# Kernel optimization log

Measured on AMD Instinct MI355X. Metric: run time of the kernel, lower is better.

## Reference

```python
import jax, jax.numpy as jnp
import numpy as np

N = 50000      # nodes
E = 400000     # edges (before self-loops)
IN = 128       # in_channels
H = 4          # heads
C = 64         # hidden_channels == out_channels (per head)
ELI = 200000   # link-prediction query edges
NEG_SLOPE = 0.2
EPS = 1e-5


def setup_inputs():
    key = jax.random.key(0)
    ks = jax.random.split(key, 20)
    sc = 0.05
    inp = {}
    inp["x"] = jax.random.normal(ks[0], (N, IN), jnp.float32)
    inp["edge_index"] = jax.random.randint(ks[1], (2, E), 0, N)
    inp["edge_label_index"] = jax.random.randint(ks[2], (2, ELI), 0, N)
    # layer 1 GATv2 params
    inp["Wl1"] = jax.random.normal(ks[3], (IN, H * C), jnp.float32) * sc
    inp["bl1"] = jnp.zeros((H * C,), jnp.float32)
    inp["Wr1"] = jax.random.normal(ks[4], (IN, H * C), jnp.float32) * sc
    inp["br1"] = jnp.zeros((H * C,), jnp.float32)
    inp["att1"] = jax.random.normal(ks[5], (H, C), jnp.float32) * sc
    inp["bias1"] = jnp.zeros((C,), jnp.float32)
    # norm1 (BatchNorm affine)
    inp["g1"] = jnp.ones((C,), jnp.float32)
    inp["b1"] = jnp.zeros((C,), jnp.float32)
    # residual projection 1 (in_channels 128 -> hidden_dim 64)
    inp["Wres"] = jax.random.normal(ks[6], (IN, C), jnp.float32) * sc
    inp["bres"] = jnp.zeros((C,), jnp.float32)
    # layer 2 GATv2 params (hidden_dim 64 -> out 64)
    inp["Wl2"] = jax.random.normal(ks[7], (C, H * C), jnp.float32) * sc
    inp["bl2"] = jnp.zeros((H * C,), jnp.float32)
    inp["Wr2"] = jax.random.normal(ks[8], (C, H * C), jnp.float32) * sc
    inp["br2"] = jnp.zeros((H * C,), jnp.float32)
    inp["att2"] = jax.random.normal(ks[9], (H, C), jnp.float32) * sc
    inp["bias2"] = jnp.zeros((C,), jnp.float32)
    # norm2
    inp["g2"] = jnp.ones((C,), jnp.float32)
    inp["b2"] = jnp.zeros((C,), jnp.float32)
    return inp


def _gatv2(x, src, dst, Wl, bl, Wr, br, att, bias, n):
    # PyG GATv2Conv, concat=False (mean over heads), dropout off (eval)
    xl = (x @ Wl + bl).reshape(n, H, -1)   # source transform
    xr = (x @ Wr + br).reshape(n, H, -1)   # target transform
    e = jax.nn.leaky_relu(xl[src] + xr[dst], NEG_SLOPE)      # [E,H,C]
    logits = jnp.einsum('ehc,hc->eh', e, att)                # [E,H]
    m = jax.ops.segment_max(logits, dst, num_segments=n)     # segment softmax
    p = jnp.exp(logits - m[dst])
    s = jax.ops.segment_sum(p, dst, num_segments=n)
    alpha = p / s[dst]                                       # [E,H]
    out = jax.ops.segment_sum(xl[src] * alpha[:, :, None], dst, num_segments=n)
    return out.mean(axis=1) + bias                           # [N,C]


def _bn(x, g, b):
    mu = x.mean(axis=0)
    var = x.var(axis=0)
    return g * (x - mu) * jax.lax.rsqrt(var + EPS) + b


def reference(x, edge_index, edge_label_index,
              Wl1, bl1, Wr1, br1, att1, bias1, g1, b1, Wres, bres,
              Wl2, bl2, Wr2, br2, att2, bias2, g2, b2):
    loop = jnp.arange(N)
    src = jnp.concatenate([edge_index[0], loop])  # add_self_loops=True
    dst = jnp.concatenate([edge_index[1], loop])
    x_res = x @ Wres + bres
    h = _gatv2(x, src, dst, Wl1, bl1, Wr1, br1, att1, bias1, N)
    h = jax.nn.relu(_bn(h, g1, b1) + x_res)
    # res_proj2 is Identity (hidden_dim == out_dim)
    h2 = _gatv2(h, src, dst, Wl2, bl2, Wr2, br2, att2, bias2, N)
    z = _bn(h2, g2, b2) + h
    scores = (z[edge_label_index[0]] * z[edge_label_index[1]]).sum(axis=-1)
    return jax.nn.sigmoid(scores)
```

## Files before the change

kernel.cpp:

```cpp
#include <hip/hip_runtime.h>
#include <math.h>

#define NN 50000
#define EE 400000
#define ETOT 450000
#define INC 128
#define CC 64
#define HC 256
#define ELI_N 200000
#define MPAD 50176

typedef unsigned short u16;
typedef __attribute__((ext_vector_type(8))) short short8v;
typedef __attribute__((ext_vector_type(8))) unsigned short u16x8;
typedef __attribute__((ext_vector_type(4))) float f32x4;
typedef __attribute__((ext_vector_type(4))) unsigned short u16x4;

__device__ __forceinline__ u16 f2b(float v){
    unsigned u = __float_as_uint(v);
    u = (u + 0x7fffu + ((u >> 16) & 1u)) >> 16;
    return (u16)u;
}
__device__ __forceinline__ float b2f(u16 h){
    return __uint_as_float(((unsigned)h) << 16);
}
__device__ __forceinline__ u16 f2h(float v){
    _Float16 h = (_Float16)v; u16 r; __builtin_memcpy(&r, &h, 2); return r;
}
__device__ __forceinline__ float h2f(u16 h){
    _Float16 x; __builtin_memcpy(&x, &h, 2); return (float)x;
}
__device__ __forceinline__ f32x4 h2f4(u16x4 r){
    f32x4 o; o[0]=h2f(r[0]); o[1]=h2f(r[1]); o[2]=h2f(r[2]); o[3]=h2f(r[3]); return o;
}

__global__ void k_setup(const float* __restrict__ x, const int* __restrict__ ei,
                        const float* __restrict__ Wl1, const float* __restrict__ Wr1,
                        const float* __restrict__ Wres, const float* __restrict__ Wl2,
                        const float* __restrict__ Wr2,
                        u16* __restrict__ xhi, u16* __restrict__ xlo,
                        u16* __restrict__ hl1, u16* __restrict__ ll1,
                        u16* __restrict__ hr1, u16* __restrict__ lr1,
                        u16* __restrict__ hres, u16* __restrict__ lres,
                        u16* __restrict__ hl2, u16* __restrict__ ll2,
                        u16* __restrict__ hr2, u16* __restrict__ lr2,
                        int* __restrict__ deg){
    int gid = blockIdx.x*256 + threadIdx.x;
    if (gid < 800000){
        int row = gid >> 4;
        int k0  = (gid & 15) * 8;
        const float* ap = x + (size_t)row*128 + k0;
        float4 v0 = *(const float4*)ap;
        float4 v1 = *(const float4*)(ap + 4);
        float vv[8] = {v0.x, v0.y, v0.z, v0.w, v1.x, v1.y, v1.z, v1.w};
        u16x8 h8, l8;
        #pragma unroll
        for (int j = 0; j < 8; j++){
            u16 h = f2b(vv[j]);
            h8[j] = h;
            l8[j] = f2b(vv[j] - b2f(h));
        }
        size_t blk = (size_t)(row >> 4)*4 + (k0 >> 5);
        size_t addr = blk*512 + (size_t)((row & 15) + 16*((k0 >> 3) & 3))*8;
        *(u16x8*)(xhi + addr) = h8;
        *(u16x8*)(xlo + addr) = l8;
    } else if (gid < 906496){
        int g = gid - 800000;
        const float* src; u16* dh; u16* dl; int K, N, idx;
        if      (g <  32768){ src=Wl1;  dh=hl1;  dl=ll1;  K=128; N=256; idx=g; }
        else if (g <  65536){ src=Wr1;  dh=hr1;  dl=lr1;  K=128; N=256; idx=g-32768; }
        else if (g <  73728){ src=Wres; dh=hres; dl=lres; K=128; N=64;  idx=g-65536; }
        else if (g <  90112){ src=Wl2;  dh=hl2;  dl=ll2;  K=64;  N=256; idx=g-73728; }
        else                { src=Wr2;  dh=hr2;  dl=lr2;  K=64;  N=256; idx=g-90112; }
        int k = idx / N, n = idx - k*N;
        float v = src[idx];
        u16 h = f2b(v);
        size_t blk = (size_t)(n >> 4)*(K >> 5) + (k >> 5);
        size_t addr = blk*512 + (size_t)((n & 15) + 16*((k >> 3) & 3))*8 + (k & 7);
        dh[addr] = h;
        dl[addr] = f2b(v - b2f(h));
    } else if (gid < 1306496){
        int e = gid - 906496;
        atomicAdd(&deg[ei[EE + e]], 1);
    }
}

__global__ void k_scanA(const int* __restrict__ deg, int* __restrict__ iscan, int* __restrict__ part){
    __shared__ int sh[256];
    int tid = threadIdx.x;
    int base = blockIdx.x*1024 + tid*4;
    int v[4]; int t = 0;
    #pragma unroll
    for (int i = 0; i < 4; i++){ int idx = base + i; v[i] = (idx < NN) ? deg[idx]+1 : 0; t += v[i]; }
    sh[tid] = t; __syncthreads();
    for (int off = 1; off < 256; off <<= 1){
        int u = (tid >= off) ? sh[tid - off] : 0;
        __syncthreads();
        sh[tid] += u;
        __syncthreads();
    }
    int incl = sh[tid];
    int run = incl - t;
    #pragma unroll
    for (int i = 0; i < 4; i++){
        run += v[i];
        int idx = base + i;
        if (idx < NN) iscan[idx] = run;
    }
    if (tid == 255) part[blockIdx.x] = incl;
}

__global__ void k_scanC(const int* __restrict__ iscan, const int* __restrict__ part,
                        const int* __restrict__ deg, int* __restrict__ rowptr, int* __restrict__ cursor){
    int chunk = blockIdx.x >> 2;
    int ps = 0;
    for (int j = 0; j < chunk; j++) ps += part[j];
    int i = blockIdx.x*256 + threadIdx.x;
    if (i < NN){
        int v = iscan[i] + ps;
        rowptr[i+1] = v;
        cursor[i] = v - (deg[i]+1);
    }
    if (i == 0) rowptr[0] = 0;
}

__global__ void k_fill(const int* __restrict__ ei, int* __restrict__ cursor, int* __restrict__ csr_src){
    int idx = blockIdx.x*256 + threadIdx.x;
    if (idx >= ETOT) return;
    int s, d;
    if (idx < EE){ s = ei[idx]; d = ei[EE + idx]; }
    else         { s = idx - EE; d = s; }
    int pos = atomicAdd(&cursor[d], 1);
    csr_src[pos] = s;
}

__global__ __launch_bounds__(256) void k_gemm1(const u16* __restrict__ Ahi, const u16* __restrict__ Alo,
        const u16* __restrict__ Whl1, const u16* __restrict__ Wll1,
        const u16* __restrict__ Whr1, const u16* __restrict__ Wlr1,
        const u16* __restrict__ Whres,const u16* __restrict__ Wlres,
        const float* __restrict__ bl1, const float* __restrict__ br1, const float* __restrict__ bres,
        u16* __restrict__ xl, u16* __restrict__ xr, u16* __restrict__ xres)
{
    int b = blockIdx.x;
    int c = b & 7;
    int k = b >> 3;
    int tile = k % 9;
    int sx = c + 8*(k/9);
    if (sx >= 196) return;
    int wid = threadIdx.x >> 6, lane = threadIdx.x & 63;
    const u16 *Bh, *Bl; const float* bias; u16* Cout; int n0, N;
    if (tile < 4)      { Bh=Whl1;  Bl=Wll1;  bias=bl1;  Cout=xl;   n0=tile*64;     N=256; }
    else if (tile < 8) { Bh=Whr1;  Bl=Wlr1;  bias=br1;  Cout=xr;   n0=(tile-4)*64; N=256; }
    else               { Bh=Whres; Bl=Wlres; bias=bres; Cout=xres; n0=0;           N=64;  }
    int rm0 = (sx*4 + wid) * 64;
    int rblk0 = rm0 >> 4;
    int nblk0 = n0 >> 4;
    int lr = lane & 15;
    f32x4 acc[4][4] = {};
    #pragma unroll
    for (int ks = 0; ks < 4; ks++){
        short8v ah[4], al[4], bh[4], blo[4];
        #pragma unroll
        for (int mf = 0; mf < 4; mf++){
            size_t addr = ((size_t)(rblk0 + mf)*4 + ks)*512 + (size_t)lane*8;
            ah[mf] = *(const short8v*)(Ahi + addr);
            al[mf] = *(const short8v*)(Alo + addr);
        }
        #pragma unroll
        for (int nf = 0; nf < 4; nf++){
            size_t addr = ((size_t)(nblk0 + nf)*4 + ks)*512 + (size_t)lane*8;
            bh[nf]  = *(const short8v*)(Bh + addr);
            blo[nf] = *(const short8v*)(Bl + addr);
        }
        #pragma unroll
        for (int mf = 0; mf < 4; mf++)
            #pragma unroll
            for (int nf = 0; nf < 4; nf++){
                acc[mf][nf] = __builtin_amdgcn_mfma_f32_16x16x32_bf16(ah[mf], bh[nf],  acc[mf][nf], 0, 0, 0);
                acc[mf][nf] = __builtin_amdgcn_mfma_f32_16x16x32_bf16(al[mf], bh[nf],  acc[mf][nf], 0, 0, 0);
                acc[mf][nf] = __builtin_amdgcn_mfma_f32_16x16x32_bf16(ah[mf], blo[nf], acc[mf][nf], 0, 0, 0);
            }
    }
    int rbase = (lane >> 4) << 2;
    #pragma unroll
    for (int nf = 0; nf < 4; nf++){
        int col = n0 + nf*16 + lr;
        float bv = bias[col];
        #pragma unroll
        for (int mf = 0; mf < 4; mf++){
            #pragma unroll
            for (int r = 0; r < 4; r++){
                int row = rm0 + mf*16 + rbase + r;
                if (row < NN) Cout[(size_t)row*N + col] = f2h(acc[mf][nf][r] + bv);
            }
        }
    }
}

__global__ __launch_bounds__(256) void k_gemm2(const u16* __restrict__ Ahi, const u16* __restrict__ Alo,
        const u16* __restrict__ Whl2, const u16* __restrict__ Wll2,
        const u16* __restrict__ Whr2, const u16* __restrict__ Wlr2,
        const float* __restrict__ bl2, const float* __restrict__ br2,
        u16* __restrict__ xl, u16* __restrict__ xr)
{
    int b = blockIdx.x;
    int c = b & 7;
    int k = b >> 3;
    int tile = k & 7;
    int sx = c + 8*(k >> 3);
    if (sx >= 196) return;
    int wid = threadIdx.x >> 6, lane = threadIdx.x & 63;
    const u16 *Bh, *Bl; const float* bias; u16* Cout;
    if (tile < 4){ Bh=Whl2; Bl=Wll2; bias=bl2; Cout=xl; }
    else         { Bh=Whr2; Bl=Wlr2; bias=br2; Cout=xr; }
    int n0 = (tile & 3)*64;
    int rm0 = (sx*4 + wid) * 64;
    int rblk0 = rm0 >> 4;
    int nblk0 = n0 >> 4;
    int lr = lane & 15;
    f32x4 acc[4][4] = {};
    #pragma unroll
    for (int ks = 0; ks < 2; ks++){
        short8v ah[4], al[4], bh[4], blo[4];
        #pragma unroll
        for (int mf = 0; mf < 4; mf++){
            size_t addr = ((size_t)(rblk0 + mf)*2 + ks)*512 + (size_t)lane*8;
            ah[mf] = *(const short8v*)(Ahi + addr);
            al[mf] = *(const short8v*)(Alo + addr);
        }
        #pragma unroll
        for (int nf = 0; nf < 4; nf++){
            size_t addr = ((size_t)(nblk0 + nf)*2 + ks)*512 + (size_t)lane*8;
            bh[nf]  = *(const short8v*)(Bh + addr);
            blo[nf] = *(const short8v*)(Bl + addr);
        }
        #pragma unroll
        for (int mf = 0; mf < 4; mf++)
            #pragma unroll
            for (int nf = 0; nf < 4; nf++){
                acc[mf][nf] = __builtin_amdgcn_mfma_f32_16x16x32_bf16(ah[mf], bh[nf],  acc[mf][nf], 0, 0, 0);
                acc[mf][nf] = __builtin_amdgcn_mfma_f32_16x16x32_bf16(al[mf], bh[nf],  acc[mf][nf], 0, 0, 0);
                acc[mf][nf] = __builtin_amdgcn_mfma_f32_16x16x32_bf16(ah[mf], blo[nf], acc[mf][nf], 0, 0, 0);
            }
    }
    int rbase = (lane >> 4) << 2;
    #pragma unroll
    for (int nf = 0; nf < 4; nf++){
        int col = n0 + nf*16 + lr;
        float bv = bias[col];
        #pragma unroll
        for (int mf = 0; mf < 4; mf++){
            #pragma unroll
            for (int r = 0; r < 4; r++){
                int row = rm0 + mf*16 + rbase + r;
                if (row < NN) Cout[(size_t)row*256 + col] = f2h(acc[mf][nf][r] + bv);
            }
        }
    }
}

__global__ __launch_bounds__(256) void k_gat(const u16* __restrict__ xl, const u16* __restrict__ xr,
                                             const int* __restrict__ csr_src, const int* __restrict__ rowptr,
                                             const float* __restrict__ att, const float* __restrict__ bias,
                                             float* __restrict__ out,
                                             float* __restrict__ part_s, float* __restrict__ part_q)
{
    __shared__ float ls[4][64];
    __shared__ float lq[4][64];
    int wave = threadIdx.x >> 6, lane = threadIdx.x & 63;
    int node = blockIdx.x*4 + wave;
    int p0 = rowptr[node], p1 = rowptr[node+1];
    f32x4 xrf  = h2f4(*(const u16x4*)(xr + (size_t)node*HC + 4*lane));
    f32x4 attf = *(const f32x4*)(att + 4*lane);
    float s = 0.f;
    f32x4 acc = {0.f, 0.f, 0.f, 0.f};
    int p = p0;
    for (; p + 4 <= p1; p += 4){
        int i0 = csr_src[p], i1 = csr_src[p+1], i2 = csr_src[p+2], i3 = csr_src[p+3];
        f32x4 x0 = h2f4(*(const u16x4*)(xl + (size_t)i0*HC + 4*lane));
        f32x4 x1 = h2f4(*(const u16x4*)(xl + (size_t)i1*HC + 4*lane));
        f32x4 x2 = h2f4(*(const u16x4*)(xl + (size_t)i2*HC + 4*lane));
        f32x4 x3 = h2f4(*(const u16x4*)(xl + (size_t)i3*HC + 4*lane));
        float t0 = 0.f, t1 = 0.f, t2 = 0.f, t3 = 0.f;
        #pragma unroll
        for (int j = 0; j < 4; j++){
            float e0 = x0[j] + xrf[j]; e0 = (e0 > 0.f) ? e0 : 0.2f*e0; t0 += e0*attf[j];
            float e1 = x1[j] + xrf[j]; e1 = (e1 > 0.f) ? e1 : 0.2f*e1; t1 += e1*attf[j];
            float e2 = x2[j] + xrf[j]; e2 = (e2 > 0.f) ? e2 : 0.2f*e2; t2 += e2*attf[j];
            float e3 = x3[j] + xrf[j]; e3 = (e3 > 0.f) ? e3 : 0.2f*e3; t3 += e3*attf[j];
        }
        #pragma unroll
        for (int off = 1; off < 16; off <<= 1){
            t0 += __shfl_xor(t0, off, 64);
            t1 += __shfl_xor(t1, off, 64);
            t2 += __shfl_xor(t2, off, 64);
            t3 += __shfl_xor(t3, off, 64);
        }
        float w0 = __expf(t0), w1 = __expf(t1), w2 = __expf(t2), w3 = __expf(t3);
        s += (w0 + w1) + (w2 + w3);
        acc = acc + x0*w0 + x1*w1 + x2*w2 + x3*w3;
    }
    for (; p < p1; p++){
        int i0 = csr_src[p];
        f32x4 x0 = h2f4(*(const u16x4*)(xl + (size_t)i0*HC + 4*lane));
        float t0 = 0.f;
        #pragma unroll
        for (int j = 0; j < 4; j++){ float e0 = x0[j] + xrf[j]; e0 = (e0 > 0.f) ? e0 : 0.2f*e0; t0 += e0*attf[j]; }
        #pragma unroll
        for (int off = 1; off < 16; off <<= 1) t0 += __shfl_xor(t0, off, 64);
        float w0 = __expf(t0);
        s += w0;
        acc = acc + x0*w0;
    }
    float inv = 1.f / s;
    f32x4 o = acc * inv;
    #pragma unroll
    for (int j = 0; j < 4; j++){ o[j] += __shfl_xor(o[j], 16, 64); o[j] += __shfl_xor(o[j], 32, 64); }
    if (lane < 16){
        f32x4 bv = *(const f32x4*)(bias + 4*lane);
        f32x4 res = o*0.25f + bv;
        *(f32x4*)(out + (size_t)node*CC + 4*lane) = res;
        #pragma unroll
        for (int j = 0; j < 4; j++){
            ls[wave][4*lane + j] = res[j];
            lq[wave][4*lane + j] = res[j]*res[j];
        }
    }
    __syncthreads();
    int tid = threadIdx.x;
    if (tid < 128){
        int c = tid & 63;
        if (tid < 64){
            float v = (ls[0][c] + ls[1][c]) + (ls[2][c] + ls[3][c]);
            atomicAdd(&part_s[(blockIdx.x & 63)*64 + c], v);
        } else {
            float v = (lq[0][c] + lq[1][c]) + (lq[2][c] + lq[3][c]);
            atomicAdd(&part_q[(blockIdx.x & 63)*64 + c], v);
        }
    }
}

__global__ __launch_bounds__(256) void k_post1(const float* __restrict__ hraw, const u16* __restrict__ xres,
                        const float* __restrict__ part_s, const float* __restrict__ part_q,
                        const float* __restrict__ g, const float* __restrict__ b,
                        float* __restrict__ out, u16* __restrict__ hhi, u16* __restrict__ hlo){
    __shared__ float red[128];
    int tid = threadIdx.x;
    if (tid < 128){
        const float* base = (tid < 64) ? part_s : part_q;
        int c = tid & 63;
        float sv = 0.f;
        for (int bb = 0; bb < 64; bb++) sv += base[bb*64 + c];
        red[tid] = sv;
    }
    __syncthreads();
    int i = blockIdx.x*256 + tid;
    if (i >= NN*16) return;
    float4 hv = ((const float4*)hraw)[i];
    f32x4 rp = h2f4(*(const u16x4*)(xres + (size_t)i*4));
    int row = i >> 4;
    int c0 = (i & 15) * 4;
    float hp[4] = {hv.x, hv.y, hv.z, hv.w};
    float res[4];
    u16x4 h4, l4;
    const float invN = 1.f / (float)NN;
    #pragma unroll
    for (int k = 0; k < 4; k++){
        int c = c0 + k;
        float mean = red[c] * invN;
        float var  = red[64 + c] * invN - mean*mean;
        float rstd = rsqrtf(var + 1e-5f);
        float v = g[c]*(hp[k] - mean)*rstd + b[c] + rp[k];
        v = (v > 0.f) ? v : 0.f;
        res[k] = v;
        u16 h = f2b(v);
        h4[k] = h;
        l4[k] = f2b(v - b2f(h));
    }
    ((float4*)out)[i] = make_float4(res[0], res[1], res[2], res[3]);
    size_t blk = (size_t)(row >> 4)*2 + (c0 >> 5);
    size_t addr = blk*512 + (size_t)((row & 15) + 16*((c0 >> 3) & 3))*8 + (c0 & 7);
    *(u16x4*)(hhi + addr) = h4;
    *(u16x4*)(hlo + addr) = l4;
}

__global__ __launch_bounds__(256) void k_post2(const float* __restrict__ hraw, const float* __restrict__ hprev,
                        const float* __restrict__ part_s, const float* __restrict__ part_q,
                        const float* __restrict__ g, const float* __restrict__ b,
                        u16* __restrict__ zout){
    __shared__ float red[128];
    int tid = threadIdx.x;
    if (tid < 128){
        const float* base = (tid < 64) ? part_s : part_q;
        int c = tid & 63;
        float sv = 0.f;
        for (int bb = 0; bb < 64; bb++) sv += base[bb*64 + c];
        red[tid] = sv;
    }
    __syncthreads();
    int i = blockIdx.x*256 + tid;
    if (i >= NN*16) return;
    float4 hv = ((const float4*)hraw)[i];
    float4 rv = ((const float4*)hprev)[i];
    int c0 = (i & 15) * 4;
    float hp[4] = {hv.x, hv.y, hv.z, hv.w};
    float rp[4] = {rv.x, rv.y, rv.z, rv.w};
    u16x4 res;
    const float invN = 1.f / (float)NN;
    #pragma unroll
    for (int k = 0; k < 4; k++){
        int c = c0 + k;
        float mean = red[c] * invN;
        float var  = red[64 + c] * invN - mean*mean;
        float rstd = rsqrtf(var + 1e-5f);
        res[k] = f2h(g[c]*(hp[k] - mean)*rstd + b[c] + rp[k]);
    }
    *(u16x4*)(zout + (size_t)i*4) = res;
}

__global__ __launch_bounds__(256) void k_score(const u16* __restrict__ z, const int* __restrict__ eli,
                                               float* __restrict__ out){
    int t = blockIdx.x*256 + threadIdx.x;
    int i = t >> 4; int j = t & 15;
    if (i >= ELI_N) return;
    int a = eli[i], b = eli[ELI_N + i];
    f32x4 va = h2f4(*(const u16x4*)(z + (size_t)a*64 + j*4));
    f32x4 vb = h2f4(*(const u16x4*)(z + (size_t)b*64 + j*4));
    float s = va[0]*vb[0] + va[1]*vb[1] + va[2]*vb[2] + va[3]*vb[3];
    #pragma unroll
    for (int off = 8; off > 0; off >>= 1) s += __shfl_xor(s, off, 64);
    if (j == 0) out[i] = 1.f / (1.f + __expf(-s));
}

extern "C" void kernel_launch(void* const* d_in, const int* in_sizes, int n_in,
                              void* d_out, int out_size, void* d_ws, size_t ws_size,
                              hipStream_t stream) {
    const float* x    = (const float*)d_in[0];
    const int*   ei   = (const int*)  d_in[1];
    const int*   eli  = (const int*)  d_in[2];
    const float* Wl1  = (const float*)d_in[3];
    const float* bl1  = (const float*)d_in[4];
    const float* Wr1  = (const float*)d_in[5];
    const float* br1  = (const float*)d_in[6];
    const float* att1 = (const float*)d_in[7];
    const float* bias1= (const float*)d_in[8];
    const float* g1   = (const float*)d_in[9];
    const float* b1   = (const float*)d_in[10];
    const float* Wres = (const float*)d_in[11];
    const float* bres = (const float*)d_in[12];
    const float* Wl2  = (const float*)d_in[13];
    const float* bl2  = (const float*)d_in[14];
    const float* Wr2  = (const float*)d_in[15];
    const float* br2  = (const float*)d_in[16];
    const float* att2 = (const float*)d_in[17];
    const float* bias2= (const float*)d_in[18];
    const float* g2   = (const float*)d_in[19];
    const float* b2   = (const float*)d_in[20];
    float* out = (float*)d_out;

    char* w = (char*)d_ws;
    size_t o = 0;
    auto take = [&](size_t bytes)->char*{ char* p = w + o; o += (bytes + 255) & ~(size_t)255; return p; };
    u16*  xl   = (u16*) take((size_t)NN*HC*2);
    u16*  xr   = (u16*) take((size_t)NN*HC*2);
    u16*  xres = (u16*) take((size_t)NN*CC*2);
    float* hraw = (float*)take((size_t)NN*CC*4);
    float* hbuf = (float*)take((size_t)NN*CC*4);
    u16*  z16  = (u16*) take((size_t)NN*CC*2);
    u16*  xhi  = (u16*)take((size_t)MPAD*INC*2);
    u16*  xlo  = (u16*)take((size_t)MPAD*INC*2);
    u16*  hhi  = (u16*)take((size_t)MPAD*CC*2);
    u16*  hlo  = (u16*)take((size_t)MPAD*CC*2);
    u16* whl1 = (u16*)take(256*128*2);  u16* wll1 = (u16*)take(256*128*2);
    u16* whr1 = (u16*)take(256*128*2);  u16* wlr1 = (u16*)take(256*128*2);
    u16* whres= (u16*)take(64*128*2);   u16* wlres= (u16*)take(64*128*2);
    u16* whl2 = (u16*)take(256*64*2);   u16* wll2 = (u16*)take(256*64*2);
    u16* whr2 = (u16*)take(256*64*2);   u16* wlr2 = (u16*)take(256*64*2);
    char* zreg  = take(4*64*64*4 + (size_t)NN*4);
    float* ps1  = (float*)zreg;
    float* pq1  = ps1 + 4096;
    float* ps2  = ps1 + 8192;
    float* pq2  = ps1 + 12288;
    int* deg    = (int*)(zreg + 4*64*64*4);
    int* rowptr = (int*)take((size_t)(NN+1)*4);
    int* iscan  = (int*)take((size_t)NN*4);
    int* cursor = (int*)take((size_t)NN*4);
    int* csr_src= (int*)take((size_t)ETOT*4);
    int* part   = (int*)take(64*4);

    hipMemsetAsync(zreg, 0, 4*64*64*4 + (size_t)NN*4, stream);

    k_setup<<<5104, 256, 0, stream>>>(x, ei, Wl1, Wr1, Wres, Wl2, Wr2,
                                      xhi, xlo,
                                      whl1, wll1, whr1, wlr1, whres, wlres,
                                      whl2, wll2, whr2, wlr2, deg);

    k_scanA<<<49, 256, 0, stream>>>(deg, iscan, part);
    k_scanC<<<196, 256, 0, stream>>>(iscan, part, deg, rowptr, cursor);
    k_fill<<<(ETOT+255)/256, 256, 0, stream>>>(ei, cursor, csr_src);

    k_gemm1<<<1800, 256, 0, stream>>>(xhi, xlo, whl1, wll1, whr1, wlr1, whres, wlres,
                                      bl1, br1, bres, xl, xr, xres);
    k_gat<<<NN/4, 256, 0, stream>>>(xl, xr, csr_src, rowptr, att1, bias1, hraw, ps1, pq1);
    k_post1<<<(NN*16+255)/256, 256, 0, stream>>>(hraw, xres, ps1, pq1, g1, b1, hbuf, hhi, hlo);

    k_gemm2<<<1600, 256, 0, stream>>>(hhi, hlo, whl2, wll2, whr2, wlr2, bl2, br2, xl, xr);
    k_gat<<<NN/4, 256, 0, stream>>>(xl, xr, csr_src, rowptr, att2, bias2, hraw, ps2, pq2);
    k_post2<<<(NN*16+255)/256, 256, 0, stream>>>(hraw, hbuf, ps2, pq2, g2, b2, z16);

    k_score<<<(ELI_N*16+255)/256, 256, 0, stream>>>(z16, eli, out);
}
```

Baseline: 289.1 us.

## Stage GEMM epilogue through LDS for vector stores; store residual h as 16-bit

Both GEMM kernels now write their 64x64 output tiles into a padded per-wave shared-memory buffer, then read them back and write 16-byte rows to global memory. This replaces scattered 2-byte stores and is meant to improve store coalescing. Separately, the layer-1 activation kept as the residual for layer 2 is stored as 16-bit instead of fp32, halving that buffer's write and read traffic at some cost in residual precision. The staging buffer adds about 40KB of LDS per block, which may reduce occupancy.

```diff
diff --git a/kernel.cpp b/kernel.cpp
--- a/kernel.cpp
+++ b/kernel.cpp
@@ -134,6 +134,8 @@
     csr_src[pos] = s;
 }
 
+#define LSTR 80
+
 __global__ __launch_bounds__(256) void k_gemm1(const u16* __restrict__ Ahi, const u16* __restrict__ Alo,
         const u16* __restrict__ Whl1, const u16* __restrict__ Wll1,
         const u16* __restrict__ Whr1, const u16* __restrict__ Wlr1,
@@ -141,6 +143,7 @@
         const float* __restrict__ bl1, const float* __restrict__ br1, const float* __restrict__ bres,
         u16* __restrict__ xl, u16* __restrict__ xr, u16* __restrict__ xres)
 {
+    __shared__ u16 stg[4][64*LSTR];
     int b = blockIdx.x;
     int c = b & 7;
     int k = b >> 3;
@@ -182,18 +185,28 @@
             }
     }
     int rbase = (lane >> 4) << 2;
+    u16* my = &stg[wid][0];
     #pragma unroll
     for (int nf = 0; nf < 4; nf++){
-        int col = n0 + nf*16 + lr;
-        float bv = bias[col];
+        int col = nf*16 + lr;
+        float bv = bias[n0 + col];
         #pragma unroll
         for (int mf = 0; mf < 4; mf++){
             #pragma unroll
             for (int r = 0; r < 4; r++){
-                int row = rm0 + mf*16 + rbase + r;
-                if (row < NN) Cout[(size_t)row*N + col] = f2h(acc[mf][nf][r] + bv);
+                int row = mf*16 + rbase + r;
+                my[row*LSTR + col] = f2h(acc[mf][nf][r] + bv);
             }
         }
+    }
+    __syncthreads();
+    int rl = lane >> 3, cl = lane & 7;
+    #pragma unroll
+    for (int it = 0; it < 8; it++){
+        int row = it*8 + rl;
+        u16x8 v = *(u16x8*)&my[row*LSTR + cl*8];
+        int grow = rm0 + row;
+        if (grow < NN) *(u16x8*)(Cout + (size_t)grow*N + n0 + cl*8) = v;
     }
 }
 
@@ -203,6 +216,7 @@
         const float* __restrict__ bl2, const float* __restrict__ br2,
         u16* __restrict__ xl, u16* __restrict__ xr)
 {
+    __shared__ u16 stg[4][64*LSTR];
     int b = blockIdx.x;
     int c = b & 7;
     int k = b >> 3;
@@ -244,18 +258,28 @@
             }
     }
     int rbase = (lane >> 4) << 2;
+    u16* my = &stg[wid][0];
     #pragma unroll
     for (int nf = 0; nf < 4; nf++){
-        int col = n0 + nf*16 + lr;
-        float bv = bias[col];
+        int col = nf*16 + lr;
+        float bv = bias[n0 + col];
         #pragma unroll
         for (int mf = 0; mf < 4; mf++){
             #pragma unroll
             for (int r = 0; r < 4; r++){
-                int row = rm0 + mf*16 + rbase + r;
-                if (row < NN) Cout[(size_t)row*256 + col] = f2h(acc[mf][nf][r] + bv);
+                int row = mf*16 + rbase + r;
+                my[row*LSTR + col] = f2h(acc[mf][nf][r] + bv);
             }
         }
+    }
+    __syncthreads();
+    int rl = lane >> 3, cl = lane & 7;
+    #pragma unroll
+    for (int it = 0; it < 8; it++){
+        int row = it*8 + rl;
+        u16x8 v = *(u16x8*)&my[row*LSTR + cl*8];
+        int grow = rm0 + row;
+        if (grow < NN) *(u16x8*)(Cout + (size_t)grow*256 + n0 + cl*8) = v;
     }
 }
 
@@ -343,7 +367,7 @@
 __global__ __launch_bounds__(256) void k_post1(const float* __restrict__ hraw, const u16* __restrict__ xres,
                         const float* __restrict__ part_s, const float* __restrict__ part_q,
                         const float* __restrict__ g, const float* __restrict__ b,
-                        float* __restrict__ out, u16* __restrict__ hhi, u16* __restrict__ hlo){
+                        u16* __restrict__ h16, u16* __restrict__ hhi, u16* __restrict__ hlo){
     __shared__ float red[128];
     int tid = threadIdx.x;
     if (tid < 128){
@@ -361,8 +385,7 @@
     int row = i >> 4;
     int c0 = (i & 15) * 4;
     float hp[4] = {hv.x, hv.y, hv.z, hv.w};
-    float res[4];
-    u16x4 h4, l4;
+    u16x4 h4, l4, hh4;
     const float invN = 1.f / (float)NN;
     #pragma unroll
     for (int k = 0; k < 4; k++){
@@ -372,19 +395,19 @@
         float rstd = rsqrtf(var + 1e-5f);
         float v = g[c]*(hp[k] - mean)*rstd + b[c] + rp[k];
         v = (v > 0.f) ? v : 0.f;
-        res[k] = v;
+        hh4[k] = f2h(v);
         u16 h = f2b(v);
         h4[k] = h;
         l4[k] = f2b(v - b2f(h));
     }
-    ((float4*)out)[i] = make_float4(res[0], res[1], res[2], res[3]);
+    *(u16x4*)(h16 + (size_t)i*4) = hh4;
     size_t blk = (size_t)(row >> 4)*2 + (c0 >> 5);
     size_t addr = blk*512 + (size_t)((row & 15) + 16*((c0 >> 3) & 3))*8 + (c0 & 7);
     *(u16x4*)(hhi + addr) = h4;
     *(u16x4*)(hlo + addr) = l4;
 }
 
-__global__ __launch_bounds__(256) void k_post2(const float* __restrict__ hraw, const float* __restrict__ hprev,
+__global__ __launch_bounds__(256) void k_post2(const float* __restrict__ hraw, const u16* __restrict__ h16,
                         const float* __restrict__ part_s, const float* __restrict__ part_q,
                         const float* __restrict__ g, const float* __restrict__ b,
                         u16* __restrict__ zout){
@@ -401,10 +424,9 @@
     int i = blockIdx.x*256 + tid;
     if (i >= NN*16) return;
     float4 hv = ((const float4*)hraw)[i];
-    float4 rv = ((const float4*)hprev)[i];
+    f32x4 rp = h2f4(*(const u16x4*)(h16 + (size_t)i*4));
     int c0 = (i & 15) * 4;
     float hp[4] = {hv.x, hv.y, hv.z, hv.w};
-    float rp[4] = {rv.x, rv.y, rv.z, rv.w};
     u16x4 res;
     const float invN = 1.f / (float)NN;
     #pragma unroll
@@ -465,7 +487,7 @@
     u16*  xr   = (u16*) take((size_t)NN*HC*2);
     u16*  xres = (u16*) take((size_t)NN*CC*2);
     float* hraw = (float*)take((size_t)NN*CC*4);
-    float* hbuf = (float*)take((size_t)NN*CC*4);
+    u16*  h16  = (u16*) take((size_t)NN*CC*2);
     u16*  z16  = (u16*) take((size_t)NN*CC*2);
     u16*  xhi  = (u16*)take((size_t)MPAD*INC*2);
     u16*  xlo  = (u16*)take((size_t)MPAD*INC*2);
@@ -502,11 +524,11 @@
     k_gemm1<<<1800, 256, 0, stream>>>(xhi, xlo, whl1, wll1, whr1, wlr1, whres, wlres,
                                       bl1, br1, bres, xl, xr, xres);
     k_gat<<<NN/4, 256, 0, stream>>>(xl, xr, csr_src, rowptr, att1, bias1, hraw, ps1, pq1);
-    k_post1<<<(NN*16+255)/256, 256, 0, stream>>>(hraw, xres, ps1, pq1, g1, b1, hbuf, hhi, hlo);
+    k_post1<<<(NN*16+255)/256, 256, 0, stream>>>(hraw, xres, ps1, pq1, g1, b1, h16, hhi, hlo);
 
     k_gemm2<<<1600, 256, 0, stream>>>(hhi, hlo, whl2, wll2, whr2, wlr2, bl2, br2, xl, xr);
     k_gat<<<NN/4, 256, 0, stream>>>(xl, xr, csr_src, rowptr, att2, bias2, hraw, ps2, pq2);
-    k_post2<<<(NN*16+255)/256, 256, 0, stream>>>(hraw, hbuf, ps2, pq2, g2, b2, z16);
+    k_post2<<<(NN*16+255)/256, 256, 0, stream>>>(hraw, h16, ps2, pq2, g2, b2, z16);
 
     k_score<<<(ELI_N*16+255)/256, 256, 0, stream>>>(z16, eli, out);
 }
```

Result: faster. 248.5 us (-14.0%).
